# Performance work log

Hardware: AMD Instinct MI355X
Metric: run time of the kernel (lower is better)

Reference implementation:

```python
import jax, jax.numpy as jnp
import numpy as np

EPS = 1e-12
ATTEND_SCALE = 8.0

def _l2norm(t, axis=-1):
    n = jnp.sqrt(jnp.sum(t * t, axis=axis, keepdims=True))
    return t / jnp.maximum(n, EPS)

def setup_inputs() -> dict:
    key = jax.random.key(0)
    k1, k2, k3, k4 = jax.random.split(key, 4)
    b, n, dim = 4, 8192, 1024
    heads, dim_head = 16, 64
    dim_inner = heads * dim_head
    x = jax.random.normal(k1, (b, n, dim), dtype=jnp.float32)
    gamma = jnp.ones((dim,), dtype=jnp.float32)  # RMSNorm gamma
    # torch Linear(dim, 3*dim_inner, bias=False): store as [dim, 3*dim_inner] for x @ W
    w_qkv = jax.random.normal(k2, (dim, 3 * dim_inner), dtype=jnp.float32) * (dim ** -0.5)
    temperature = jnp.zeros((heads, 1, 1), dtype=jnp.float32)
    w_out = jax.random.normal(k3, (dim_inner, dim), dtype=jnp.float32) * (dim_inner ** -0.5)
    return {"x": x, "gamma": gamma, "w_qkv": w_qkv, "temperature": temperature, "w_out": w_out}

def reference(x, gamma, w_qkv, temperature, w_out):
    b, n, dim = x.shape
    heads = temperature.shape[0]
    dim_head = w_qkv.shape[1] // (3 * heads)
    # RMSNorm: F.normalize(x, dim=-1) * sqrt(dim) * gamma
    xn = _l2norm(x) * (dim ** 0.5) * gamma
    qkv = xn @ w_qkv  # [b, n, 3*h*d]
    qkv = qkv.reshape(b, n, 3, heads, dim_head).transpose(2, 0, 3, 4, 1)  # [3, b, h, d, n]
    q, k, v = qkv[0], qkv[1], qkv[2]
    orig_v = v
    # l2-normalize q, k over the sequence axis (last dim of [b,h,d,n])
    q = _l2norm(q) * jnp.exp(temperature)  # temperature [h,1,1] broadcasts
    k = _l2norm(k)
    # attention over the feature axis: sim [b, h, d, d]
    sim = jnp.einsum('bhdn,bhen->bhde', q, k) * ATTEND_SCALE
    attn = jax.nn.softmax(sim, axis=-1)
    out = jnp.einsum('bhde,bhen->bhdn', attn, v)  # [b, h, d, n]
    out = out.transpose(0, 3, 1, 2).reshape(b, n, heads * dim_head) @ w_out  # [b, n, dim]
    return out, orig_v
```

## Files before the change

### kernel.cpp

```cpp
#include <hip/hip_runtime.h>
#include <hip/hip_bf16.h>

#define DEVI __device__ __forceinline__

using bf16x8 = __attribute__((ext_vector_type(8))) __bf16;
using f32x4  = __attribute__((ext_vector_type(4))) float;
using u16x8  = __attribute__((ext_vector_type(8))) unsigned short;

DEVI unsigned short f2bf(float f) {
  unsigned int u = __float_as_uint(f);
  u = (u + 0x7FFFu + ((u >> 16) & 1u)) >> 16;
  return (unsigned short)u;
}
DEVI float bf2f(unsigned short s) { return __uint_as_float(((unsigned int)s) << 16); }

DEVI void gld_lds16(const unsigned short* g, unsigned short* l) {
  __builtin_amdgcn_global_load_lds(
      (const __attribute__((address_space(1))) void*)g,
      (__attribute__((address_space(3))) void*)l, 16, 0, 0);
}

__global__ __launch_bounds__(256) void transpose_cast_kernel(const float* __restrict__ in,
                                                             unsigned short* __restrict__ out,
                                                             int R, int C) {
  __shared__ float tile[32][33];
  const int c0 = blockIdx.x * 32, r0 = blockIdx.y * 32;
  const int tx = threadIdx.x & 31, ty = threadIdx.x >> 5;
  for (int rr = ty; rr < 32; rr += 8)
    tile[rr][tx] = in[(size_t)(r0 + rr) * C + c0 + tx];
  __syncthreads();
  for (int cc = ty; cc < 32; cc += 8)
    out[(size_t)(c0 + cc) * R + r0 + tx] = f2bf(tile[tx][cc]);
}

__global__ __launch_bounds__(256) void castv_kernel(const float* __restrict__ w_qkv,
                                                    unsigned short* __restrict__ Wv_nt) {
  const int i = blockIdx.x * 256 + threadIdx.x;
  const int k = i >> 8, he4 = (i & 255) * 4;
  const float4 v = *(const float4*)&w_qkv[(size_t)k * 3072 + 2048 + he4];
  ushort4 o;
  o.x = f2bf(v.x); o.y = f2bf(v.y); o.z = f2bf(v.z); o.w = f2bf(v.w);
  *(ushort4*)&Wv_nt[(size_t)k * 1024 + he4] = o;
}

__global__ __launch_bounds__(256) void transpose_bf16_kernel(const unsigned short* __restrict__ in,
                                                             unsigned short* __restrict__ out,
                                                             int R, int C) {
  __shared__ unsigned short tile[32][33];
  const int c0 = blockIdx.x * 32, r0 = blockIdx.y * 32;
  const int tx = threadIdx.x & 31, ty = threadIdx.x >> 5;
  for (int rr = ty; rr < 32; rr += 8)
    tile[rr][tx] = in[(size_t)(r0 + rr) * C + c0 + tx];
  __syncthreads();
  for (int cc = ty; cc < 32; cc += 8)
    out[(size_t)(c0 + cc) * R + r0 + tx] = tile[tx][cc];
}

__global__ __launch_bounds__(256) void rmsnorm_kernel(const float* __restrict__ x,
                                                      const float* __restrict__ gamma,
                                                      unsigned short* __restrict__ xn) {
  __shared__ float wsum[4];
  const int row = blockIdx.x;
  const int t = threadIdx.x;
  const float4 v = *(const float4*)&x[(size_t)row * 1024 + t * 4];
  float s = v.x * v.x + v.y * v.y + v.z * v.z + v.w * v.w;
  for (int off = 32; off; off >>= 1) s += __shfl_down(s, off);
  if ((t & 63) == 0) wsum[t >> 6] = s;
  __syncthreads();
  const float tot = wsum[0] + wsum[1] + wsum[2] + wsum[3];
  const float scale = 32.0f / fmaxf(sqrtf(tot), 1e-12f);
  const float4 g = *(const float4*)&gamma[t * 4];
  ushort4 o;
  o.x = f2bf(v.x * scale * g.x);
  o.y = f2bf(v.y * scale * g.y);
  o.z = f2bf(v.z * scale * g.z);
  o.w = f2bf(v.w * scale * g.w);
  *(ushort4*)&xn[(size_t)row * 1024 + t * 4] = o;
}

__global__ __launch_bounds__(256) void gemm_gram_kernel(const unsigned short* __restrict__ xnT,
                                                        unsigned short* __restrict__ Gp) {
  if (blockIdx.x > blockIdx.y) return;
  __shared__ __align__(16) unsigned short Al[4096];
  __shared__ __align__(16) unsigned short Bl[4096];
  const int tid = threadIdx.x;
  const int lane = tid & 63, wid = tid >> 6;
  const int wr = wid >> 1, wc = wid & 1;
  const int r = lane & 15, kg = lane >> 4;
  const int rw0 = tid >> 2, q0 = (tid & 3) * 8;
  const size_t row0 = (size_t)blockIdx.y * 128, col0 = (size_t)blockIdx.x * 128;
  const int z = blockIdx.z;
  const size_t koff = (size_t)(z >> 2) * 8192 + (size_t)(z & 3) * 2048;
  f32x4 acc[4][4] = {};
  for (int k0 = 0; k0 < 2048; k0 += 32) {
    __syncthreads();
    gld_lds16(&xnT[(row0 + rw0) * 32768 + koff + k0 + q0], &Al[tid * 8]);
    gld_lds16(&xnT[(row0 + rw0 + 64) * 32768 + koff + k0 + q0], &Al[2048 + tid * 8]);
    gld_lds16(&xnT[(col0 + rw0) * 32768 + koff + k0 + q0], &Bl[tid * 8]);
    gld_lds16(&xnT[(col0 + rw0 + 64) * 32768 + koff + k0 + q0], &Bl[2048 + tid * 8]);
    __syncthreads();
    bf16x8 af[4], bfr[4];
#pragma unroll
    for (int m = 0; m < 4; ++m) af[m] = *(const bf16x8*)&Al[(wr * 64 + m * 16 + r) * 32 + kg * 8];
#pragma unroll
    for (int n = 0; n < 4; ++n) bfr[n] = *(const bf16x8*)&Bl[(wc * 64 + n * 16 + r) * 32 + kg * 8];
#pragma unroll
    for (int m = 0; m < 4; ++m)
#pragma unroll
      for (int n = 0; n < 4; ++n)
        acc[m][n] = __builtin_amdgcn_mfma_f32_16x16x32_bf16(af[m], bfr[n], acc[m][n], 0, 0, 0);
  }
  unsigned short* C = Gp + ((size_t)z << 20);
  const int rbase = wr * 64 + (lane >> 4) * 4;
  const int cbase = wc * 64 + (lane & 15);
#pragma unroll
  for (int m = 0; m < 4; ++m)
#pragma unroll
    for (int n = 0; n < 4; ++n)
#pragma unroll
      for (int j = 0; j < 4; ++j)
        C[(row0 + rbase + m * 16 + j) * 1024 + col0 + cbase + n * 16] = f2bf(acc[m][n][j]);
}

__global__ __launch_bounds__(256) void greduce_kernel(const unsigned short* __restrict__ Gp,
                                                      unsigned short* __restrict__ G) {
  const int tj = blockIdx.x, ti = blockIdx.y, b = blockIdx.z;
  if ((tj >> 1) > (ti >> 1)) return;
  __shared__ float lds[64][65];
  const int t = threadIdx.x;
  const int r = t >> 2, c0 = (t & 3) * 16;
  const size_t idx = (size_t)(ti * 64 + r) * 1024 + tj * 64 + c0;
  float v[16];
#pragma unroll
  for (int j = 0; j < 16; ++j) v[j] = 0.f;
  for (int s = 0; s < 4; ++s) {
    const unsigned short* p = Gp + ((size_t)(b * 4 + s) << 20) + idx;
#pragma unroll
    for (int j = 0; j < 16; ++j) v[j] += bf2f(p[j]);
  }
  unsigned short* Gb = G + ((size_t)b << 20);
  __attribute__((aligned(16))) unsigned short buf[16];
#pragma unroll
  for (int j = 0; j < 16; ++j) buf[j] = f2bf(v[j]);
  { int4* dst = (int4*)&Gb[idx]; const int4* src = (const int4*)buf; dst[0] = src[0]; dst[1] = src[1]; }
  if ((ti >> 1) != (tj >> 1)) {
#pragma unroll
    for (int j = 0; j < 16; ++j) lds[r][c0 + j] = v[j];
    __syncthreads();
    const int x = t >> 2, y0 = (t & 3) * 16;
#pragma unroll
    for (int j = 0; j < 16; ++j) buf[j] = f2bf(lds[y0 + j][x]);
    int4* dst = (int4*)&Gb[(size_t)(tj * 64 + x) * 1024 + ti * 64 + y0];
    const int4* src = (const int4*)buf;
    dst[0] = src[0]; dst[1] = src[1];
  }
}

__global__ __launch_bounds__(256) void gemm_bt_batch_bf16(const unsigned short* __restrict__ A,
                                                          const unsigned short* __restrict__ Bt,
                                                          unsigned short* __restrict__ C,
                                                          int N, int K,
                                                          long long aStr, long long bStr, long long cStr) {
  __shared__ __align__(16) unsigned short Al[4096];
  __shared__ __align__(16) unsigned short Bl[4096];
  A += (size_t)blockIdx.z * aStr; Bt += (size_t)blockIdx.z * bStr; C += (size_t)blockIdx.z * cStr;
  const int tid = threadIdx.x;
  const int lane = tid & 63, wid = tid >> 6;
  const int wr = wid >> 1, wc = wid & 1;
  const int r = lane & 15, kg = lane >> 4;
  const int rw0 = tid >> 2, q0 = (tid & 3) * 8;
  const size_t row0 = (size_t)blockIdx.y * 128, col0 = (size_t)blockIdx.x * 128;
  f32x4 acc[4][4] = {};
  for (int k0 = 0; k0 < K; k0 += 32) {
    __syncthreads();
    gld_lds16(&A[(row0 + rw0) * K + k0 + q0], &Al[tid * 8]);
    gld_lds16(&A[(row0 + rw0 + 64) * K + k0 + q0], &Al[2048 + tid * 8]);
    gld_lds16(&Bt[(col0 + rw0) * K + k0 + q0], &Bl[tid * 8]);
    gld_lds16(&Bt[(col0 + rw0 + 64) * K + k0 + q0], &Bl[2048 + tid * 8]);
    __syncthreads();
    bf16x8 af[4], bfr[4];
#pragma unroll
    for (int m = 0; m < 4; ++m) af[m] = *(const bf16x8*)&Al[(wr * 64 + m * 16 + r) * 32 + kg * 8];
#pragma unroll
    for (int n = 0; n < 4; ++n) bfr[n] = *(const bf16x8*)&Bl[(wc * 64 + n * 16 + r) * 32 + kg * 8];
#pragma unroll
    for (int m = 0; m < 4; ++m)
#pragma unroll
      for (int n = 0; n < 4; ++n)
        acc[m][n] = __builtin_amdgcn_mfma_f32_16x16x32_bf16(af[m], bfr[n], acc[m][n], 0, 0, 0);
  }
  const int rbase = wr * 64 + (lane >> 4) * 4;
  const int cbase = wc * 64 + (lane & 15);
#pragma unroll
  for (int m = 0; m < 4; ++m)
#pragma unroll
    for (int n = 0; n < 4; ++n)
#pragma unroll
      for (int j = 0; j < 4; ++j)
        C[(row0 + rbase + m * 16 + j) * N + col0 + cbase + n * 16] = f2bf(acc[m][n][j]);
}

__global__ __launch_bounds__(256) void gemm_vout_kernel(const unsigned short* __restrict__ A,
                                                        const unsigned short* __restrict__ BtV,
                                                        const unsigned short* __restrict__ WfoldT,
                                                        float* __restrict__ origv,
                                                        float* __restrict__ outp) {
  __shared__ __align__(16) unsigned short Al[4096];
  __shared__ __align__(16) unsigned short Bl[4096];
  const int flat = blockIdx.x;
  const int s = (flat & 7) * 512 + (flat >> 3);
  const int cb = s & 15, rb = s >> 4;
  const size_t row0 = (size_t)rb * 128;
  const int b = rb >> 6;
  const unsigned short* Bt = (cb < 8)
      ? BtV + (size_t)cb * 128 * 1024
      : WfoldT + ((size_t)b << 20) + (size_t)(cb - 8) * 128 * 1024;
  const int tid = threadIdx.x;
  const int lane = tid & 63, wid = tid >> 6;
  const int wr = wid >> 1, wc = wid & 1;
  const int r = lane & 15, kg = lane >> 4;
  const int rw0 = tid >> 2, q0 = (tid & 3) * 8;
  const int K = 1024;
  f32x4 acc[4][4] = {};
  for (int k0 = 0; k0 < K; k0 += 32) {
    __syncthreads();
    gld_lds16(&A[(row0 + rw0) * K + k0 + q0], &Al[tid * 8]);
    gld_lds16(&A[(row0 + rw0 + 64) * K + k0 + q0], &Al[2048 + tid * 8]);
    gld_lds16(&Bt[(size_t)rw0 * K + k0 + q0], &Bl[tid * 8]);
    gld_lds16(&Bt[(size_t)(rw0 + 64) * K + k0 + q0], &Bl[2048 + tid * 8]);
    __syncthreads();
    bf16x8 af[4], bfr[4];
#pragma unroll
    for (int m = 0; m < 4; ++m) af[m] = *(const bf16x8*)&Al[(wr * 64 + m * 16 + r) * 32 + kg * 8];
#pragma unroll
    for (int n = 0; n < 4; ++n) bfr[n] = *(const bf16x8*)&Bl[(wc * 64 + n * 16 + r) * 32 + kg * 8];
#pragma unroll
    for (int m = 0; m < 4; ++m)
#pragma unroll
      for (int n = 0; n < 4; ++n)
        acc[m][n] = __builtin_amdgcn_mfma_f32_16x16x32_bf16(af[m], bfr[n], acc[m][n], 0, 0, 0);
  }
  const int rbase = wr * 64 + (lane >> 4) * 4;
  const int cbase = wc * 64 + (lane & 15);
  if (cb < 8) {
    const int nn0 = (int)(row0 & 8191) + rbase;
#pragma unroll
    for (int m = 0; m < 4; ++m)
#pragma unroll
      for (int n = 0; n < 4; ++n) {
        const int hd = cb * 128 + cbase + n * 16;
        float4 o4;
        o4.x = acc[m][n][0]; o4.y = acc[m][n][1]; o4.z = acc[m][n][2]; o4.w = acc[m][n][3];
        *(float4*)&origv[((size_t)b * 1024 + hd) * 8192 + nn0 + m * 16] = o4;
      }
  } else {
    const size_t col0 = (size_t)(cb - 8) * 128;
#pragma unroll
    for (int m = 0; m < 4; ++m)
#pragma unroll
      for (int n = 0; n < 4; ++n)
#pragma unroll
        for (int j = 0; j < 4; ++j)
          outp[(row0 + rbase + m * 16 + j) * 1024 + col0 + cbase + n * 16] = acc[m][n][j];
  }
}

__global__ __launch_bounds__(256) void norms_kernel(const unsigned short* __restrict__ UTt,
                                                    const unsigned short* __restrict__ wqkvT,
                                                    float* __restrict__ qkn2) {
  const int t = threadIdx.x;
  const int rloc = t >> 4, lane16 = t & 15;
  const int row = blockIdx.x * 16 + rloc;
  const int b = row >> 11, r2 = row & 2047;
  const unsigned short* pa = UTt + ((size_t)b << 21) + (size_t)r2 * 1024 + lane16 * 64;
  const unsigned short* pb = wqkvT + (size_t)r2 * 1024 + lane16 * 64;
  float s = 0.f;
  for (int i = 0; i < 64; i += 8) {
    const u16x8 va = *(const u16x8*)&pa[i];
    const u16x8 vb = *(const u16x8*)&pb[i];
#pragma unroll
    for (int j = 0; j < 8; ++j) s += bf2f(va[j]) * bf2f(vb[j]);
  }
  for (int off = 8; off; off >>= 1) s += __shfl_down(s, off, 16);
  if (lane16 == 0) qkn2[row] = s;
}

__global__ __launch_bounds__(256) void sim_softmax_kernel(const unsigned short* __restrict__ wqkvT,
                                                          const unsigned short* __restrict__ UTt,
                                                          const float* __restrict__ qkn2,
                                                          const float* __restrict__ temperature,
                                                          float* __restrict__ attn) {
  __shared__ __align__(16) unsigned short Aql[64 * 128];
  __shared__ __align__(16) unsigned short Bkl[64 * 128];
  __shared__ float qknl[2][64];
  const int bh = blockIdx.x;
  const int b = bh >> 4, h = bh & 15;
  const int t = threadIdx.x;
  const int lane = t & 63, w = t >> 6;
  const unsigned short* UTtb = UTt + ((size_t)b << 21);
  if (t < 128) {
    const int sel = t >> 6, dd = t & 63;
    qknl[sel][dd] = fmaxf(sqrtf(qkn2[b * 2048 + sel * 1024 + h * 64 + dd]), 1e-12f);
  }
  const unsigned short* AqG = UTtb + (size_t)(h * 64) * 1024;
  const unsigned short* BkG = wqkvT + (size_t)(1024 + h * 64) * 1024;
  const int r = lane & 15, kg = lane >> 4;
  const int srow = t >> 4, scol = (t & 15) * 8;
  f32x4 acc[4] = {};
  for (int k0 = 0; k0 < 1024; k0 += 128) {
    __syncthreads();
#pragma unroll
    for (int c = 0; c < 4; ++c) {
      gld_lds16(&AqG[(size_t)(c * 16 + srow) * 1024 + k0 + scol], &Aql[c * 2048 + t * 8]);
      gld_lds16(&BkG[(size_t)(c * 16 + srow) * 1024 + k0 + scol], &Bkl[c * 2048 + t * 8]);
    }
    __syncthreads();
#pragma unroll
    for (int kk = 0; kk < 128; kk += 32) {
      const bf16x8 af = *(const bf16x8*)&Aql[(w * 16 + r) * 128 + kk + kg * 8];
#pragma unroll
      for (int n = 0; n < 4; ++n) {
        const bf16x8 bfr = *(const bf16x8*)&Bkl[(n * 16 + r) * 128 + kk + kg * 8];
        acc[n] = __builtin_amdgcn_mfma_f32_16x16x32_bf16(af, bfr, acc[n], 0, 0, 0);
      }
    }
  }
  const float sc = 8.f * __expf(temperature[h]);
  const int colq = lane & 15, rq = lane >> 4;
#pragma unroll
  for (int j = 0; j < 4; ++j) {
    const int d = w * 16 + rq * 4 + j;
    const float qd = qknl[0][d];
    float sv[4];
#pragma unroll
    for (int n = 0; n < 4; ++n) sv[n] = acc[n][j] * sc / (qd * qknl[1][n * 16 + colq]);
    float mj = fmaxf(fmaxf(sv[0], sv[1]), fmaxf(sv[2], sv[3]));
    for (int msk = 1; msk < 16; msk <<= 1) mj = fmaxf(mj, __shfl_xor(mj, msk));
    float p[4], sum = 0.f;
#pragma unroll
    for (int n = 0; n < 4; ++n) { p[n] = __expf(sv[n] - mj); sum += p[n]; }
    for (int msk = 1; msk < 16; msk <<= 1) sum += __shfl_xor(sum, msk);
    const float inv = 1.f / sum;
#pragma unroll
    for (int n = 0; n < 4; ++n)
      attn[(size_t)bh * 4096 + d * 64 + n * 16 + colq] = p[n] * inv;
  }
}

__global__ __launch_bounds__(256) void w2t_kernel(const float* __restrict__ attn,
                                                  const float* __restrict__ w_out,
                                                  unsigned short* __restrict__ W2T) {
  __shared__ float al[64][64];
  __shared__ float wl[64][64];
  const int bh = blockIdx.y;
  const int b = bh >> 4, h = bh & 15;
  const int c0 = blockIdx.x * 256;
  const int t = threadIdx.x, e = t & 63, g = t >> 6;
  const int dr = t >> 2, q4 = (t & 3) * 16;
#pragma unroll
  for (int j = 0; j < 16; j += 4)
    *(float4*)&al[dr][q4 + j] = *(const float4*)&attn[(size_t)bh * 4096 + dr * 64 + q4 + j];
  for (int cb = 0; cb < 4; ++cb) {
    __syncthreads();
#pragma unroll
    for (int j = 0; j < 16; j += 4)
      *(float4*)&wl[dr][q4 + j] = *(const float4*)&w_out[(size_t)(h * 64 + dr) * 1024 + c0 + cb * 64 + q4 + j];
    __syncthreads();
#pragma unroll
    for (int i = 0; i < 16; ++i) {
      const int cc = g * 16 + i;
      float s = 0.f;
#pragma unroll 8
      for (int d = 0; d < 64; ++d) s += al[d][e] * wl[d][cc];
      W2T[((size_t)b << 20) + (size_t)(c0 + cb * 64 + cc) * 1024 + h * 64 + e] = f2bf(s);
    }
  }
}

extern "C" void kernel_launch(void* const* d_in, const int* in_sizes, int n_in,
                              void* d_out, int out_size, void* d_ws, size_t ws_size,
                              hipStream_t stream) {
  const float* x     = (const float*)d_in[0];
  const float* gamma = (const float*)d_in[1];
  const float* w_qkv = (const float*)d_in[2];
  const float* temp  = (const float*)d_in[3];
  const float* w_out = (const float*)d_in[4];
  char* ws = (char*)d_ws;
  unsigned short* wqkvT  = (unsigned short*)(ws);
  unsigned short* Wv_nt  = (unsigned short*)(ws + 6291456);
  unsigned short* xn     = (unsigned short*)(ws + 8388608);
  unsigned short* xnT    = (unsigned short*)(ws + 75497472);
  unsigned short* Gp     = (unsigned short*)(ws + 142606336);
  unsigned short* G      = (unsigned short*)(ws + 176160768);
  unsigned short* UTt    = (unsigned short*)(ws + 184549376);
  float* qkn2            = (float*)(ws + 201326592);
  float* attn            = (float*)(ws + 201359360);
  unsigned short* W2T    = (unsigned short*)(ws + 202407936);
  unsigned short* WfoldT = (unsigned short*)(ws + 210796544);
  float* outp  = (float*)d_out;
  float* origv = outp + (size_t)33554432;

  transpose_cast_kernel<<<dim3(96, 32), 256, 0, stream>>>(w_qkv, wqkvT, 1024, 3072);
  castv_kernel<<<1024, 256, 0, stream>>>(w_qkv, Wv_nt);
  rmsnorm_kernel<<<32768, 256, 0, stream>>>(x, gamma, xn);
  transpose_bf16_kernel<<<dim3(32, 1024), 256, 0, stream>>>(xn, xnT, 32768, 1024);
  gemm_gram_kernel<<<dim3(8, 8, 16), 256, 0, stream>>>(xnT, Gp);
  greduce_kernel<<<dim3(16, 16, 4), 256, 0, stream>>>(Gp, G);
  gemm_bt_batch_bf16<<<dim3(8, 16, 4), 256, 0, stream>>>(wqkvT, G, UTt, 1024, 1024,
                                                         0LL, 1LL << 20, 1LL << 21);
  norms_kernel<<<512, 256, 0, stream>>>(UTt, wqkvT, qkn2);
  sim_softmax_kernel<<<64, 256, 0, stream>>>(wqkvT, UTt, qkn2, temp, attn);
  w2t_kernel<<<dim3(4, 64), 256, 0, stream>>>(attn, w_out, W2T);
  gemm_bt_batch_bf16<<<dim3(8, 8, 4), 256, 0, stream>>>(W2T, Wv_nt, WfoldT, 1024, 1024,
                                                        1LL << 20, 0LL, 1LL << 20);
  gemm_vout_kernel<<<4096, 256, 0, stream>>>(xn, wqkvT + (size_t)2048 * 1024, WfoldT,
                                             origv, outp);
}
```

Measured before the change: 550.9 us.

## Enlarge final GEMM tile to 256x256 with double-buffered swizzled LDS pipeline

Replaces the 128x128 single-buffered final GEMM (which produces V and the output) with a 512-thread, 256x256-tile kernel. It stages K in blocks of 64, double-buffers LDS, uses an XOR-swizzled layout and explicit vmcnt waits, so global loads overlap MFMA compute and each loaded element is reused more. The bf16 transpose of the normalized input also moves to 64x64 tiles with 4-wide vector loads and stores. The larger tile uses far more LDS and registers, which lowers occupancy and leaves fewer blocks to fill the GPU.

Measured after the change: 510.8 us. -7.3%, faster.

```diff
diff --git a/kernel.cpp b/kernel.cpp
--- a/kernel.cpp
+++ b/kernel.cpp
@@ -43,17 +43,29 @@
   *(ushort4*)&Wv_nt[(size_t)k * 1024 + he4] = o;
 }
 
-__global__ __launch_bounds__(256) void transpose_bf16_kernel(const unsigned short* __restrict__ in,
-                                                             unsigned short* __restrict__ out,
-                                                             int R, int C) {
-  __shared__ unsigned short tile[32][33];
-  const int c0 = blockIdx.x * 32, r0 = blockIdx.y * 32;
-  const int tx = threadIdx.x & 31, ty = threadIdx.x >> 5;
-  for (int rr = ty; rr < 32; rr += 8)
-    tile[rr][tx] = in[(size_t)(r0 + rr) * C + c0 + tx];
+__global__ __launch_bounds__(256) void transpose_bf16x4_kernel(const unsigned short* __restrict__ in,
+                                                               unsigned short* __restrict__ out) {
+  __shared__ unsigned short tile[64][68];
+  const int r0 = blockIdx.x * 64;
+  const int c0 = blockIdx.y * 64;
+  const int t = threadIdx.x;
+  const int tr = t >> 4, tc4 = (t & 15) * 4;
+#pragma unroll
+  for (int p = 0; p < 4; ++p) {
+    const int rr = p * 16 + tr;
+    *(ushort4*)&tile[rr][tc4] = *(const ushort4*)&in[(size_t)(r0 + rr) * 1024 + c0 + tc4];
+  }
   __syncthreads();
-  for (int cc = ty; cc < 32; cc += 8)
-    out[(size_t)(c0 + cc) * R + r0 + tx] = tile[tx][cc];
+#pragma unroll
+  for (int p = 0; p < 4; ++p) {
+    const int cc = p * 16 + tr;
+    ushort4 o;
+    o.x = tile[tc4 + 0][cc];
+    o.y = tile[tc4 + 1][cc];
+    o.z = tile[tc4 + 2][cc];
+    o.w = tile[tc4 + 3][cc];
+    *(ushort4*)&out[(size_t)(c0 + cc) * 32768 + r0 + tc4] = o;
+  }
 }
 
 __global__ __launch_bounds__(256) void rmsnorm_kernel(const float* __restrict__ x,
@@ -200,68 +212,119 @@
         C[(row0 + rbase + m * 16 + j) * N + col0 + cbase + n * 16] = f2bf(acc[m][n][j]);
 }
 
-__global__ __launch_bounds__(256) void gemm_vout_kernel(const unsigned short* __restrict__ A,
-                                                        const unsigned short* __restrict__ BtV,
-                                                        const unsigned short* __restrict__ WfoldT,
-                                                        float* __restrict__ origv,
-                                                        float* __restrict__ outp) {
-  __shared__ __align__(16) unsigned short Al[4096];
-  __shared__ __align__(16) unsigned short Bl[4096];
-  const int flat = blockIdx.x;
-  const int s = (flat & 7) * 512 + (flat >> 3);
-  const int cb = s & 15, rb = s >> 4;
-  const size_t row0 = (size_t)rb * 128;
-  const int b = rb >> 6;
-  const unsigned short* Bt = (cb < 8)
-      ? BtV + (size_t)cb * 128 * 1024
-      : WfoldT + ((size_t)b << 20) + (size_t)(cb - 8) * 128 * 1024;
-  const int tid = threadIdx.x;
-  const int lane = tid & 63, wid = tid >> 6;
-  const int wr = wid >> 1, wc = wid & 1;
+DEVI void stage256(const unsigned short* __restrict__ gA,
+                   const unsigned short* __restrict__ gB,
+                   unsigned short* lA, unsigned short* lB,
+                   int k0, int w, int lane) {
+  const int dr = lane >> 3;
+  const int ks = (lane & 7) ^ dr;
+  const size_t lo = (size_t)dr * 1024 + k0 + ks * 8;
+#pragma unroll
+  for (int i = 0; i < 4; ++i) {
+    const int oct = w * 4 + i;
+    gld_lds16(gA + (size_t)oct * 8192 + lo, lA + oct * 512 + lane * 8);
+    gld_lds16(gB + (size_t)oct * 8192 + lo, lB + oct * 512 + lane * 8);
+  }
+}
+
+DEVI void compute256(const unsigned short* __restrict__ lA,
+                     const unsigned short* __restrict__ lB,
+                     int wm, int wn, int lane, f32x4 (&acc)[8][4]) {
   const int r = lane & 15, kg = lane >> 4;
-  const int rw0 = tid >> 2, q0 = (tid & 3) * 8;
-  const int K = 1024;
-  f32x4 acc[4][4] = {};
-  for (int k0 = 0; k0 < K; k0 += 32) {
-    __syncthreads();
-    gld_lds16(&A[(row0 + rw0) * K + k0 + q0], &Al[tid * 8]);
-    gld_lds16(&A[(row0 + rw0 + 64) * K + k0 + q0], &Al[2048 + tid * 8]);
-    gld_lds16(&Bt[(size_t)rw0 * K + k0 + q0], &Bl[tid * 8]);
-    gld_lds16(&Bt[(size_t)(rw0 + 64) * K + k0 + q0], &Bl[2048 + tid * 8]);
-    __syncthreads();
-    bf16x8 af[4], bfr[4];
-#pragma unroll
-    for (int m = 0; m < 4; ++m) af[m] = *(const bf16x8*)&Al[(wr * 64 + m * 16 + r) * 32 + kg * 8];
-#pragma unroll
-    for (int n = 0; n < 4; ++n) bfr[n] = *(const bf16x8*)&Bl[(wc * 64 + n * 16 + r) * 32 + kg * 8];
-#pragma unroll
-    for (int m = 0; m < 4; ++m)
+  const int r7 = r & 7;
+#pragma unroll
+  for (int ksl = 0; ksl < 2; ++ksl) {
+    const int sA = (((ksl << 2) + kg) ^ r7) * 8;
+    bf16x8 af[8], bfr[4];
+#pragma unroll
+    for (int m = 0; m < 8; ++m)
+      af[m] = *(const bf16x8*)&lA[(wm * 128 + m * 16 + r) * 64 + sA];
+#pragma unroll
+    for (int n = 0; n < 4; ++n)
+      bfr[n] = *(const bf16x8*)&lB[(wn * 64 + n * 16 + r) * 64 + sA];
+#pragma unroll
+    for (int m = 0; m < 8; ++m)
 #pragma unroll
       for (int n = 0; n < 4; ++n)
         acc[m][n] = __builtin_amdgcn_mfma_f32_16x16x32_bf16(af[m], bfr[n], acc[m][n], 0, 0, 0);
   }
-  const int rbase = wr * 64 + (lane >> 4) * 4;
-  const int cbase = wc * 64 + (lane & 15);
-  if (cb < 8) {
-    const int nn0 = (int)(row0 & 8191) + rbase;
-#pragma unroll
-    for (int m = 0; m < 4; ++m)
+}
+
+#define VOUT_BAR()  __builtin_amdgcn_sched_barrier(0); __builtin_amdgcn_s_barrier(); \
+                    __builtin_amdgcn_sched_barrier(0)
+#define VOUT_W8()   asm volatile("s_waitcnt vmcnt(8)" ::: "memory")
+#define VOUT_W0()   asm volatile("s_waitcnt vmcnt(0)" ::: "memory")
+
+__global__ __launch_bounds__(512, 2) void gemm_vout256_kernel(
+    const unsigned short* __restrict__ A,
+    const unsigned short* __restrict__ BtV,
+    const unsigned short* __restrict__ WfoldT,
+    float* __restrict__ origv,
+    float* __restrict__ outp) {
+  __shared__ __align__(16) unsigned short Al[2][16384];
+  __shared__ __align__(16) unsigned short Bl[2][16384];
+  const int tid = threadIdx.x;
+  const int lane = tid & 63;
+  const int w = tid >> 6;
+  const int wm = w >> 2, wn = w & 3;
+  const int cb = blockIdx.x & 7;
+  const int rb = blockIdx.x >> 3;
+  const int b = rb >> 5;
+  const unsigned short* gA = A + (size_t)rb * 256 * 1024;
+  const unsigned short* gB = (cb < 4)
+      ? BtV + (size_t)cb * 256 * 1024
+      : WfoldT + ((size_t)b << 20) + (size_t)(cb - 4) * 256 * 1024;
+
+  f32x4 acc[8][4] = {};
+  stage256(gA, gB, Al[0], Bl[0], 0, w, lane);
+#pragma unroll 1
+  for (int tt = 0; tt < 7; ++tt) {
+    stage256(gA, gB, Al[1], Bl[1], (tt * 2 + 1) * 64, w, lane);
+    VOUT_W8(); VOUT_BAR();
+    __builtin_amdgcn_s_setprio(1);
+    compute256(Al[0], Bl[0], wm, wn, lane, acc);
+    __builtin_amdgcn_s_setprio(0);
+    VOUT_BAR();
+    stage256(gA, gB, Al[0], Bl[0], (tt * 2 + 2) * 64, w, lane);
+    VOUT_W8(); VOUT_BAR();
+    __builtin_amdgcn_s_setprio(1);
+    compute256(Al[1], Bl[1], wm, wn, lane, acc);
+    __builtin_amdgcn_s_setprio(0);
+    VOUT_BAR();
+  }
+  stage256(gA, gB, Al[1], Bl[1], 15 * 64, w, lane);
+  VOUT_W8(); VOUT_BAR();
+  __builtin_amdgcn_s_setprio(1);
+  compute256(Al[0], Bl[0], wm, wn, lane, acc);
+  __builtin_amdgcn_s_setprio(0);
+  VOUT_BAR();
+  VOUT_W0(); VOUT_BAR();
+  __builtin_amdgcn_s_setprio(1);
+  compute256(Al[1], Bl[1], wm, wn, lane, acc);
+  __builtin_amdgcn_s_setprio(0);
+
+  const int rr = (lane >> 4) * 4;
+  const int cc = lane & 15;
+  if (cb < 4) {
+    const int nbase = (rb & 31) * 256 + wm * 128;
+#pragma unroll
+    for (int m = 0; m < 8; ++m)
 #pragma unroll
       for (int n = 0; n < 4; ++n) {
-        const int hd = cb * 128 + cbase + n * 16;
-        float4 o4;
-        o4.x = acc[m][n][0]; o4.y = acc[m][n][1]; o4.z = acc[m][n][2]; o4.w = acc[m][n][3];
-        *(float4*)&origv[((size_t)b * 1024 + hd) * 8192 + nn0 + m * 16] = o4;
+        const int hd = cb * 256 + wn * 64 + n * 16 + cc;
+        const float4 o4 = make_float4(acc[m][n][0], acc[m][n][1], acc[m][n][2], acc[m][n][3]);
+        *(float4*)&origv[((size_t)b * 1024 + hd) * 8192 + nbase + m * 16 + rr] = o4;
       }
   } else {
-    const size_t col0 = (size_t)(cb - 8) * 128;
-#pragma unroll
-    for (int m = 0; m < 4; ++m)
+    const size_t grow0 = (size_t)rb * 256 + wm * 128;
+    const int gc0 = (cb - 4) * 256 + wn * 64;
+#pragma unroll
+    for (int m = 0; m < 8; ++m)
 #pragma unroll
       for (int n = 0; n < 4; ++n)
 #pragma unroll
         for (int j = 0; j < 4; ++j)
-          outp[(row0 + rbase + m * 16 + j) * 1024 + col0 + cbase + n * 16] = acc[m][n][j];
+          outp[(grow0 + m * 16 + rr + j) * 1024 + gc0 + n * 16 + cc] = acc[m][n][j];
   }
 }
 
@@ -360,11 +423,11 @@
 #pragma unroll
   for (int j = 0; j < 16; j += 4)
     *(float4*)&al[dr][q4 + j] = *(const float4*)&attn[(size_t)bh * 4096 + dr * 64 + q4 + j];
-  for (int cb = 0; cb < 4; ++cb) {
+  for (int cbk = 0; cbk < 4; ++cbk) {
     __syncthreads();
 #pragma unroll
     for (int j = 0; j < 16; j += 4)
-      *(float4*)&wl[dr][q4 + j] = *(const float4*)&w_out[(size_t)(h * 64 + dr) * 1024 + c0 + cb * 64 + q4 + j];
+      *(float4*)&wl[dr][q4 + j] = *(const float4*)&w_out[(size_t)(h * 64 + dr) * 1024 + c0 + cbk * 64 + q4 + j];
     __syncthreads();
 #pragma unroll
     for (int i = 0; i < 16; ++i) {
@@ -372,7 +435,7 @@
       float s = 0.f;
 #pragma unroll 8
       for (int d = 0; d < 64; ++d) s += al[d][e] * wl[d][cc];
-      W2T[((size_t)b << 20) + (size_t)(c0 + cb * 64 + cc) * 1024 + h * 64 + e] = f2bf(s);
+      W2T[((size_t)b << 20) + (size_t)(c0 + cbk * 64 + cc) * 1024 + h * 64 + e] = f2bf(s);
     }
   }
 }
@@ -403,7 +466,7 @@
   transpose_cast_kernel<<<dim3(96, 32), 256, 0, stream>>>(w_qkv, wqkvT, 1024, 3072);
   castv_kernel<<<1024, 256, 0, stream>>>(w_qkv, Wv_nt);
   rmsnorm_kernel<<<32768, 256, 0, stream>>>(x, gamma, xn);
-  transpose_bf16_kernel<<<dim3(32, 1024), 256, 0, stream>>>(xn, xnT, 32768, 1024);
+  transpose_bf16x4_kernel<<<dim3(512, 16), 256, 0, stream>>>(xn, xnT);
   gemm_gram_kernel<<<dim3(8, 8, 16), 256, 0, stream>>>(xnT, Gp);
   greduce_kernel<<<dim3(16, 16, 4), 256, 0, stream>>>(Gp, G);
   gemm_bt_batch_bf16<<<dim3(8, 16, 4), 256, 0, stream>>>(wqkvT, G, UTt, 1024, 1024,
@@ -413,6 +476,6 @@
   w2t_kernel<<<dim3(4, 64), 256, 0, stream>>>(attn, w_out, W2T);
   gemm_bt_batch_bf16<<<dim3(8, 8, 4), 256, 0, stream>>>(W2T, Wv_nt, WfoldT, 1024, 1024,
                                                         1LL << 20, 0LL, 1LL << 20);
-  gemm_vout_kernel<<<4096, 256, 0, stream>>>(xn, wqkvT + (size_t)2048 * 1024, WfoldT,
-                                             origv, outp);
-}
+  gemm_vout256_kernel<<<1024, 512, 0, stream>>>(xn, wqkvT + (size_t)2048 * 1024, WfoldT,
+                                                origv, outp);
+}
```
